# Performance work log

Hardware: AMD Instinct MI355X
Metric: run time of the kernel (lower is better)

The kernel has to match this reference:

```python
import jax, jax.numpy as jnp
import numpy as np

B = 128          # graphs
NPG = 512        # nodes per graph
N = B * NPG      # total nodes
DEG = 8
E = N * DEG      # total edges (intra-graph)
D = 100          # num_feature_dim / num_node_labels
HID = 128        # config.hidden
HEADS = 8
F1 = 20          # per-head dim of first GATConv in each GATNet
RATIO = 0.5
K = int(np.ceil(RATIO * NPG))  # nodes kept per graph by SAGPooling
NEG_SLOPE = 0.2


def setup_inputs() -> dict:
    key = jax.random.key(0)
    ks = jax.random.split(key, 24)
    x = jax.random.randint(ks[0], (N,), 0, D)
    # intra-graph random edges: local ids in [0, NPG) + graph offset
    src_l = jax.random.randint(ks[1], (B, NPG * DEG), 0, NPG)
    dst_l = jax.random.randint(ks[2], (B, NPG * DEG), 0, NPG)
    off = (jnp.arange(B) * NPG)[:, None]
    edge_index = jnp.stack([(src_l + off).ravel(), (dst_l + off).ravel()])
    batch = jnp.repeat(jnp.arange(B), NPG)

    def lin(k, fan_in, fan_out):
        return jax.random.normal(k, (fan_in, fan_out), jnp.float32) / np.sqrt(fan_in)

    def att(k, h, f):
        return jax.random.normal(k, (h, f), jnp.float32) * 0.1

    p = {
        # GATNet A (conv1): GATConv(D, 20, heads=8) then GATConv(160, HID, heads=1)
        "W_a1": lin(ks[3], D, HEADS * F1), "asrc_a1": att(ks[4], HEADS, F1),
        "adst_a1": att(ks[5], HEADS, F1), "b_a1": jnp.zeros((HEADS * F1,), jnp.float32),
        "W_a2": lin(ks[6], HEADS * F1, HID), "asrc_a2": att(ks[7], 1, HID),
        "adst_a2": att(ks[8], 1, HID), "b_a2": jnp.zeros((HID,), jnp.float32),
        # GATNet B (conv4): GATConv(HID, 20, heads=8) then GATConv(160, HID, heads=1)
        "W_b1": lin(ks[9], HID, HEADS * F1), "asrc_b1": att(ks[10], HEADS, F1),
        "adst_b1": att(ks[11], HEADS, F1), "b_b1": jnp.zeros((HEADS * F1,), jnp.float32),
        "W_b2": lin(ks[12], HEADS * F1, HID), "asrc_b2": att(ks[13], 1, HID),
        "adst_b2": att(ks[14], 1, HID), "b_b2": jnp.zeros((HID,), jnp.float32),
        # SAGPooling GraphConv(HID, 1)
        "w_rel": lin(ks[15], HID, 1), "w_root": lin(ks[16], HID, 1),
        "b_pool": jnp.zeros((1,), jnp.float32),
    }
    return {"x": x, "edge_index": edge_index, "batch": batch, **p}


def _gat_conv(h, src, dst, W, asrc, adst, b):
    """PyG GATConv (with self-loops already included in src/dst)."""
    Hh, Ff = asrc.shape
    z = (h @ W).reshape(N, Hh, Ff)                       # [N,H,F]
    es = jnp.sum(z * asrc, axis=-1)                      # [N,H] source logits
    ed = jnp.sum(z * adst, axis=-1)                      # [N,H] dest logits
    e = jax.nn.leaky_relu(es[src] + ed[dst], NEG_SLOPE)  # [E',H]
    m = jax.ops.segment_max(e, dst, num_segments=N)
    m = jnp.where(jnp.isfinite(m), m, 0.0)
    ex = jnp.exp(e - m[dst])
    den = jax.ops.segment_sum(ex, dst, num_segments=N)
    alpha = ex / (den[dst] + 1e-16)
    out = jax.ops.segment_sum(z[src] * alpha[:, :, None], dst, num_segments=N)
    return out.reshape(N, Hh * Ff) + b


def reference(x, edge_index, batch,
              W_a1, asrc_a1, adst_a1, b_a1, W_a2, asrc_a2, adst_a2, b_a2,
              W_b1, asrc_b1, adst_b1, b_b1, W_b2, asrc_b2, adst_b2, b_b2,
              w_rel, w_root, b_pool):
    src, dst = edge_index[0], edge_index[1]
    loops = jnp.arange(N)
    src_sl = jnp.concatenate([src, loops])  # GATConv adds self loops
    dst_sl = jnp.concatenate([dst, loops])

    h = jax.nn.one_hot(x, D, dtype=jnp.float32)
    # GATNet A: conv1 -> relu -> conv2 ; outer relu (dropout is eval no-op)
    h = jax.nn.relu(_gat_conv(h, src_sl, dst_sl, W_a1, asrc_a1, adst_a1, b_a1))
    h = _gat_conv(h, src_sl, dst_sl, W_a2, asrc_a2, adst_a2, b_a2)
    h = jax.nn.relu(h)
    # GATNet B
    h = jax.nn.relu(_gat_conv(h, src_sl, dst_sl, W_b1, asrc_b1, adst_b1, b_b1))
    h = _gat_conv(h, src_sl, dst_sl, W_b2, asrc_b2, adst_b2, b_b2)
    h = jax.nn.relu(h)

    # SAGPooling: GraphConv(HID,1) score (no self loops), tanh, per-graph top-k
    nbr = jax.ops.segment_sum(h[src], dst, num_segments=N)
    score = jnp.tanh(nbr @ w_rel + h @ w_root + b_pool).ravel()   # [N]
    sv, si = jax.lax.top_k(score.reshape(B, NPG), K)              # [B,K]
    perm = (si + (jnp.arange(B) * NPG)[:, None]).ravel()          # global node ids
    x_sel = h[perm] * sv.ravel()[:, None]                         # [B*K, HID]
    pooled = jnp.max(x_sel.reshape(B, K, HID), axis=1)            # global_max_pool
    batch_out = jnp.repeat(jnp.arange(B), K)
    return (pooled, perm, sv.ravel(), batch_out)
```

## Files before the change

kernel.cpp:

```cpp
#include <hip/hip_runtime.h>
#include <math.h>

#define N_NODES 65536
#define NPG     512
#define NGRAPH  128
#define E_EDGES 524288
#define MAXDEG  64
#define NHEADS  8
#define F1      20
#define HID     128
#define D160    160
#define KSEL    256
#define NLBL    100

#define IMG_A2_ELEMS (144*168)
#define IMG_B1_ELEMS (176*136)
#define PB_ZERO 0
#define PB_A2   64
#define PB_B1   (PB_A2 + 95)
#define PB_B2   (PB_B1 + 94)
#define PB_WA1  (PB_B2 + 95)
#define PB_EST  (PB_WA1 + 63)
#define PB_TOT  (PB_EST + 7)

typedef unsigned short ushort_t;
typedef unsigned int   uint_t;
typedef unsigned long long u64;
typedef __attribute__((ext_vector_type(8))) short short8;
typedef __attribute__((ext_vector_type(4))) float f32x4;

__device__ __forceinline__ float lrelu(float x){ return x > 0.f ? x : 0.2f*x; }
__device__ __forceinline__ ushort_t f2bf(float f){
    uint_t u = __float_as_uint(f);
    return (ushort_t)((u + 0x7FFFu + ((u >> 16) & 1u)) >> 16);
}
__device__ __forceinline__ float bf2f(ushort_t u){ return __uint_as_float(((uint_t)u) << 16); }
__device__ __forceinline__ float bflo(uint_t v){ return __uint_as_float(v << 16); }
__device__ __forceinline__ float bfhi(uint_t v){ return __uint_as_float(v & 0xFFFF0000u); }
__device__ __forceinline__ int xswz(int bid, int nblocks){
    return (bid & 7) * (nblocks >> 3) + (bid >> 3);
}
__device__ __forceinline__ float rdlanef(float v, int i){
    return __uint_as_float((uint_t)__builtin_amdgcn_readlane(__float_as_int(v), i));
}

__device__ __forceinline__ u64 comp_make(float s, int idx){
    uint_t u = __float_as_uint(s);
    u ^= (u & 0x80000000u) ? 0xFFFFFFFFu : 0x80000000u;
    return ((u64)u << 32) | (u64)(511 - idx);
}
__device__ __forceinline__ float comp_score(u64 c){
    uint_t u = (uint_t)(c >> 32);
    u ^= (u & 0x80000000u) ? 0x80000000u : 0xFFFFFFFFu;
    return __uint_as_float(u);
}
__device__ __forceinline__ int comp_idx(u64 c){ return 511 - (int)(c & 0x1FFu); }
__device__ __forceinline__ u64 shfl_xor_u64(u64 x, int m){
    uint_t lo = __shfl_xor((uint_t)x, m);
    uint_t hi = __shfl_xor((uint_t)(x >> 32), m);
    return ((u64)hi << 32) | lo;
}

__global__ void k_prep(const float* __restrict__ Wa1, const float* __restrict__ as1,
                       const float* __restrict__ ad1,
                       const float* __restrict__ Wa2, const float* __restrict__ as2,
                       const float* __restrict__ ad2,
                       const float* __restrict__ Wb1, const float* __restrict__ asb1,
                       const float* __restrict__ adb1,
                       const float* __restrict__ Wb2, const float* __restrict__ asb2,
                       const float* __restrict__ adb2,
                       int* __restrict__ deg,
                       ushort_t* __restrict__ imgA2, ushort_t* __restrict__ imgB1,
                       ushort_t* __restrict__ imgB2,
                       ushort_t* __restrict__ Wbf, float* __restrict__ esT,
                       float* __restrict__ edT){
    int bid = blockIdx.x, tid = threadIdx.x;
    if(bid < PB_A2){
        ((uint4*)deg)[(bid - PB_ZERO)*256 + tid] = (uint4){0,0,0,0};
    } else if(bid < PB_B1 || (bid >= PB_B2 && bid < PB_WA1)){
        bool isB2 = (bid >= PB_B2);
        int j = (bid - (isB2 ? PB_B2 : PB_A2))*256 + tid;
        if(j < IMG_A2_ELEMS){
            const float* W  = isB2 ? Wb2 : Wa2;
            const float* as = isB2 ? asb2 : as2;
            const float* ad = isB2 ? adb2 : ad2;
            int n = j / 168, k = j - n*168;
            float v = 0.f;
            if(k < 160){
                if(n < 128) v = W[k*128 + n];
                else if(n < 130){
                    const float* av = (n == 128) ? as : ad;
                    float s = 0.f;
                    for(int c=0; c<128; ++c) s += W[k*128 + c]*av[c];
                    v = s;
                }
            }
            (isB2 ? imgB2 : imgA2)[j] = f2bf(v);
        }
    } else if(bid < PB_B2){
        int j = (bid - PB_B1)*256 + tid;
        if(j < IMG_B1_ELEMS){
            int n = j / 136, k = j - n*136;
            float v = 0.f;
            if(k < 128){
                if(n < 160) v = Wb1[k*160 + n];
                else {
                    int j2 = n - 160, h = j2 & 7;
                    const float* av = ((j2 < 8) ? asb1 : adb1) + h*F1;
                    const float* wr = Wb1 + k*160 + h*F1;
                    float s = 0.f;
                    #pragma unroll
                    for(int f=0; f<F1; ++f) s += wr[f]*av[f];
                    v = s;
                }
            }
            imgB1[j] = f2bf(v);
        }
    } else if(bid < PB_EST){
        int j = (bid - PB_WA1)*256 + tid;
        if(j < NLBL*D160) Wbf[j] = f2bf(Wa1[j]);
    } else {
        int t = (bid - PB_EST)*256 + tid;
        if(t < NLBL*16){
            int lbl = t >> 4, j = t & 15, h = j & 7;
            const float* av = ((j < 8) ? as1 : ad1) + h*F1;
            const float* wr = Wa1 + lbl*D160 + h*F1;
            float s = 0.f;
            #pragma unroll
            for(int f=0; f<F1; ++f) s += wr[f]*av[f];
            if(j < 8) esT[lbl*8 + h] = s;
            else      edT[lbl*8 + h] = s;
        }
    }
}

__global__ void k_build_ell(const int* __restrict__ src, const int* __restrict__ dst,
                            int* __restrict__ deg, int* __restrict__ ell){
    int blk = xswz(blockIdx.x, E_EDGES/256);
    int e = blk*blockDim.x + threadIdx.x;
    int d = dst[e];
    int p = atomicAdd(&deg[d], 1);
    if(p < MAXDEG) ell[d*MAXDEG + p] = src[e];
}

__global__ __launch_bounds__(256) void k_attn8_a(const int* __restrict__ x,
        const int* __restrict__ deg, const int* __restrict__ ell,
        const ushort_t* __restrict__ Wbf, const float* __restrict__ esT,
        const float* __restrict__ edT, const float* __restrict__ bias,
        ushort_t* __restrict__ out){
    __shared__ __align__(16) ushort_t Wl[NLBL*D160];
    __shared__ float esL[NLBL*8], edL[NLBL*8];
    int tid = threadIdx.x;
    for(int i = tid; i < NLBL*D160/8; i += 256)
        ((uint4*)Wl)[i] = ((const uint4*)Wbf)[i];
    for(int i = tid; i < NLBL*8; i += 256){ esL[i] = esT[i]; edL[i] = edT[i]; }
    __syncthreads();
    int blk = xswz(blockIdx.x, N_NODES*NHEADS/256);
    int t = blk*256 + tid;
    int n = t >> 3, h = t & 7;
    int dg = deg[n]; if(dg > MAXDEG) dg = MAXDEG;
    int lbl = x[n];
    float edn = edL[lbl*8 + h];
    float wself = expf(lrelu(esL[lbl*8 + h] + edn));
    float den = wself;
    float acc[F1];
    {
        const uint_t* zn = (const uint_t*)Wl + lbl*80 + h*10;
        #pragma unroll
        for(int f=0; f<10; ++f){
            uint_t v = zn[f];
            acc[2*f]   = wself*bflo(v);
            acc[2*f+1] = wself*bfhi(v);
        }
    }
    const int* el = ell + n*MAXDEG;
    int i = 0;
    for(; i+2 <= dg; i += 2){
        int sa = el[i], sb = el[i+1];
        int la = x[sa], lb = x[sb];
        float wa = expf(lrelu(esL[la*8 + h] + edn));
        float wb = expf(lrelu(esL[lb*8 + h] + edn));
        den += wa + wb;
        const uint_t* za = (const uint_t*)Wl + la*80 + h*10;
        const uint_t* zb = (const uint_t*)Wl + lb*80 + h*10;
        #pragma unroll
        for(int f=0; f<10; ++f){
            uint_t va = za[f], vb = zb[f];
            acc[2*f]   += wa*bflo(va) + wb*bflo(vb);
            acc[2*f+1] += wa*bfhi(va) + wb*bfhi(vb);
        }
    }
    if(i < dg){
        int sa = el[i];
        int la = x[sa];
        float wa = expf(lrelu(esL[la*8 + h] + edn));
        den += wa;
        const uint_t* za = (const uint_t*)Wl + la*80 + h*10;
        #pragma unroll
        for(int f=0; f<10; ++f){
            uint_t va = za[f];
            acc[2*f]   += wa*bflo(va);
            acc[2*f+1] += wa*bfhi(va);
        }
    }
    float inv = 1.f/(den + 1e-16f);
    uint_t* o = (uint_t*)(out + (size_t)n*D160 + h*F1);
    const float* bb = bias + h*F1;
    #pragma unroll
    for(int f=0; f<10; ++f){
        float v0 = fmaxf(acc[2*f]*inv   + bb[2*f],   0.f);
        float v1 = fmaxf(acc[2*f+1]*inv + bb[2*f+1], 0.f);
        o[f] = (uint_t)f2bf(v0) | ((uint_t)f2bf(v1) << 16);
    }
}

__global__ void k_attn8(const int* __restrict__ deg, const int* __restrict__ ell,
                        const ushort_t* __restrict__ z8, const float* __restrict__ es8,
                        const float* __restrict__ ed8, const float* __restrict__ bias,
                        ushort_t* __restrict__ out){
    int blk = xswz(blockIdx.x, N_NODES*NHEADS/256);
    int t = blk*blockDim.x + threadIdx.x;
    int n = t >> 3, h = t & 7;
    int dg = deg[n]; if(dg > MAXDEG) dg = MAXDEG;
    float edn = ed8[t];
    float wself = expf(lrelu(es8[t] + edn));
    float den = wself;
    float acc[F1];
    const uint_t* zn = (const uint_t*)(z8 + (size_t)n*D160 + h*F1);
    #pragma unroll
    for(int f=0; f<10; ++f){
        uint_t v = zn[f];
        acc[2*f]   = wself*bflo(v);
        acc[2*f+1] = wself*bfhi(v);
    }
    const int* el = ell + n*MAXDEG;
    int i = 0;
    for(; i+2 <= dg; i += 2){
        int sa = el[i], sb = el[i+1];
        float ea = es8[sa*NHEADS + h], eb = es8[sb*NHEADS + h];
        const uint_t* za = (const uint_t*)(z8 + (size_t)sa*D160 + h*F1);
        const uint_t* zb = (const uint_t*)(z8 + (size_t)sb*D160 + h*F1);
        float wa = expf(lrelu(ea + edn));
        float wb = expf(lrelu(eb + edn));
        den += wa + wb;
        #pragma unroll
        for(int f=0; f<10; ++f){
            uint_t va = za[f], vb = zb[f];
            acc[2*f]   += wa*bflo(va) + wb*bflo(vb);
            acc[2*f+1] += wa*bfhi(va) + wb*bfhi(vb);
        }
    }
    if(i < dg){
        int sa = el[i];
        float ea = es8[sa*NHEADS + h];
        const uint_t* za = (const uint_t*)(z8 + (size_t)sa*D160 + h*F1);
        float wa = expf(lrelu(ea + edn));
        den += wa;
        #pragma unroll
        for(int f=0; f<10; ++f){
            uint_t va = za[f];
            acc[2*f]   += wa*bflo(va);
            acc[2*f+1] += wa*bfhi(va);
        }
    }
    float inv = 1.f/(den + 1e-16f);
    uint_t* o = (uint_t*)(out + (size_t)n*D160 + h*F1);
    const float* bb = bias + h*F1;
    #pragma unroll
    for(int f=0; f<10; ++f){
        float v0 = fmaxf(acc[2*f]*inv   + bb[2*f],   0.f);
        float v1 = fmaxf(acc[2*f+1]*inv + bb[2*f+1], 0.f);
        o[f] = (uint_t)f2bf(v0) | ((uint_t)f2bf(v1) << 16);
    }
}

template<int IN, int OUTC, int OUTIMG, bool ESED8>
__global__ __launch_bounds__(256) void k_gemm2(const ushort_t* __restrict__ Wimg,
                                               const ushort_t* __restrict__ A,
                                               ushort_t* __restrict__ C,
                                               float* __restrict__ oa,
                                               float* __restrict__ ob){
    constexpr int LDW = IN + 8;
    constexpr int NT = OUTIMG/16;
    constexpr int NC = OUTC/16;
    constexpr int KS = IN/32;
    constexpr int ELEMS = OUTIMG*LDW;
    __shared__ __align__(16) ushort_t Wt[ELEMS];
    int tid = threadIdx.x;
    int blk = xswz(blockIdx.x, N_NODES/64);
    int wave = tid >> 6, lane = tid & 63;
    int col16 = lane & 15;
    int kq = (lane >> 4) * 8;
    int row = blk*64 + wave*16 + col16;
    const ushort_t* Ar = A + (size_t)row*IN + kq;
    short8 afr[KS];
    #pragma unroll
    for(int ks=0; ks<KS; ++ks)
        afr[ks] = *reinterpret_cast<const short8*>(Ar + ks*32);
    for(int i = tid; i < ELEMS/8; i += 256)
        ((uint4*)Wt)[i] = ((const uint4*)Wimg)[i];
    __syncthreads();
    f32x4 acc[NT];
    #pragma unroll
    for(int c=0;c<NT;++c) acc[c] = (f32x4){0.f,0.f,0.f,0.f};
    #pragma unroll
    for(int ks=0; ks<KS; ++ks){
        #pragma unroll
        for(int c=0;c<NT;++c){
            short8 bf = *reinterpret_cast<const short8*>(&Wt[(c*16 + col16)*LDW + ks*32 + kq]);
            acc[c] = __builtin_amdgcn_mfma_f32_16x16x32_bf16(afr[ks], bf, acc[c], 0, 0, 0);
        }
    }
    int rbase = blk*64 + wave*16 + (lane >> 4)*4;
    #pragma unroll
    for(int c=0;c<NC;++c){
        #pragma unroll
        for(int r=0;r<4;++r){
            C[(size_t)(rbase + r)*OUTC + c*16 + col16] = f2bf(acc[c][r]);
        }
    }
    if(ESED8){
        #pragma unroll
        for(int r=0;r<4;++r){
            float v = acc[NT-1][r];
            if(col16 < 8) oa[(size_t)(rbase + r)*8 + col16] = v;
            else          ob[(size_t)(rbase + r)*8 + (col16 - 8)] = v;
        }
    } else {
        if(col16 == 0){
            #pragma unroll
            for(int r=0;r<4;++r) oa[rbase + r] = acc[NT-1][r];
        }
        if(col16 == 1){
            #pragma unroll
            for(int r=0;r<4;++r) ob[rbase + r] = acc[NT-1][r];
        }
    }
}

template<typename OutT, bool DOT>
__global__ void k_attn1(const int* __restrict__ deg, const int* __restrict__ ell,
                        const ushort_t* __restrict__ Z, const float* __restrict__ es,
                        const float* __restrict__ ed, const float* __restrict__ bias,
                        OutT* __restrict__ out,
                        const float* __restrict__ wa, const float* __restrict__ wb,
                        float* __restrict__ oa, float* __restrict__ ob){
    int blk = xswz(blockIdx.x, N_NODES/4);
    int gt = blk*blockDim.x + threadIdx.x;
    int n = gt >> 6;
    int l = threadIdx.x & 63;
    int dg = deg[n]; if(dg > MAXDEG) dg = MAXDEG;
    float edn = ed[n];
    float wself = expf(lrelu(es[n] + edn));
    int s_l = 0; float w_l = 0.f;
    if(l < dg){ s_l = ell[n*MAXDEG + l]; w_l = expf(lrelu(es[s_l] + edn)); }
    float den = w_l;
    for(int o=32;o>0;o>>=1) den += __shfl_xor(den,o);
    den += wself;
    const uint_t* Zu = (const uint_t*)Z;
    uint_t zn = Zu[(size_t)n*64 + l];
    float acc0 = wself*bflo(zn);
    float acc1 = wself*bfhi(zn);
    int i = 0;
    for(; i+4 <= dg; i += 4){
        int s0 = __builtin_amdgcn_readlane(s_l, i);
        int s1 = __builtin_amdgcn_readlane(s_l, i+1);
        int s2 = __builtin_amdgcn_readlane(s_l, i+2);
        int s3 = __builtin_amdgcn_readlane(s_l, i+3);
        uint_t z0 = Zu[(size_t)s0*64 + l];
        uint_t z1 = Zu[(size_t)s1*64 + l];
        uint_t z2 = Zu[(size_t)s2*64 + l];
        uint_t z3 = Zu[(size_t)s3*64 + l];
        float w0 = rdlanef(w_l, i);
        float w1 = rdlanef(w_l, i+1);
        float w2 = rdlanef(w_l, i+2);
        float w3 = rdlanef(w_l, i+3);
        acc0 += w0*bflo(z0) + w1*bflo(z1);
        acc1 += w0*bfhi(z0) + w1*bfhi(z1);
        acc0 += w2*bflo(z2) + w3*bflo(z3);
        acc1 += w2*bfhi(z2) + w3*bfhi(z3);
    }
    for(; i < dg; ++i){
        int s0 = __builtin_amdgcn_readlane(s_l, i);
        float w0 = rdlanef(w_l, i);
        uint_t z0 = Zu[(size_t)s0*64 + l];
        acc0 += w0*bflo(z0);
        acc1 += w0*bfhi(z0);
    }
    float inv = 1.f/(den + 1e-16f);
    float2 bb = ((const float2*)bias)[l];
    float r0 = fmaxf(acc0*inv + bb.x, 0.f);
    float r1 = fmaxf(acc1*inv + bb.y, 0.f);
    if(sizeof(OutT) == 2){
        ((uint_t*)out)[(size_t)n*64 + l] = (uint_t)f2bf(r0) | ((uint_t)f2bf(r1) << 16);
    } else {
        float2 rv; rv.x = r0; rv.y = r1;
        ((float2*)out)[(size_t)n*64 + l] = rv;
    }
    if(DOT){
        float2 a2 = ((const float2*)wa)[l];
        float2 b2 = ((const float2*)wb)[l];
        float pa = r0*a2.x + r1*a2.y;
        float pb = r0*b2.x + r1*b2.y;
        for(int o=32;o>0;o>>=1){ pa += __shfl_xor(pa,o); pb += __shfl_xor(pb,o); }
        if(l==0){ oa[n] = pa; ob[n] = pb; }
    }
}

__global__ void k_score(const int* __restrict__ deg, const int* __restrict__ ell,
                        const float* __restrict__ yrel, const float* __restrict__ rroot,
                        const float* __restrict__ bpool, float* __restrict__ score){
    int blk = xswz(blockIdx.x, N_NODES/256);
    int n = blk*blockDim.x + threadIdx.x;
    int dg = deg[n]; if(dg > MAXDEG) dg = MAXDEG;
    float s = rroot[n] + bpool[0];
    const int* el = ell + n*MAXDEG;
    int i = 0;
    for(; i+4 <= dg; i += 4){
        float y0 = yrel[el[i]],   y1 = yrel[el[i+1]];
        float y2 = yrel[el[i+2]], y3 = yrel[el[i+3]];
        s += (y0 + y1) + (y2 + y3);
    }
    for(; i < dg; ++i) s += yrel[el[i]];
    score[n] = tanhf(s);
}

__global__ __launch_bounds__(512) void k_topk_pool(const float* __restrict__ score,
                                                   const ushort_t* __restrict__ H,
                                                   float* __restrict__ pooled,
                                                   float* __restrict__ perm_f,
                                                   float* __restrict__ sv,
                                                   float* __restrict__ batch_f){
    __shared__ int   sidx[KSEL];
    __shared__ float sval[KSEL];
    __shared__ float pmax[512];
    int g = xswz(blockIdx.x, NGRAPH);
    int base = g*NPG;
    int t = threadIdx.x;
    if(t < 64){
        int l = t;
        u64 v[8];
        #pragma unroll
        for(int r=0;r<8;++r){
            int i = r*64 + l;
            v[r] = comp_make(score[base + i], i);
        }
        #pragma unroll
        for(int kk=1; kk<=9; ++kk){
            int k = 1 << kk;
            #pragma unroll
            for(int jj=kk-1; jj>=0; --jj){
                int j = 1 << jj;
                if(j < 64){
                    bool lower = (l & j) == 0;
                    #pragma unroll
                    for(int r=0;r<8;++r){
                        int i = r*64 + l;
                        u64 p = shfl_xor_u64(v[r], j);
                        bool desc = (i & k) == 0;
                        u64 mx = v[r] > p ? v[r] : p;
                        u64 mn = v[r] > p ? p : v[r];
                        v[r] = (lower == desc) ? mx : mn;
                    }
                } else {
                    int jr = j >> 6;
                    #pragma unroll
                    for(int r=0;r<8;++r){
                        if((r & jr) == 0){
                            int rp = r | jr;
                            int i = r*64 + l;
                            bool desc = (i & k) == 0;
                            u64 a = v[r], b = v[rp];
                            u64 mx = a > b ? a : b;
                            u64 mn = a > b ? b : a;
                            v[r]  = desc ? mx : mn;
                            v[rp] = desc ? mn : mx;
                        }
                    }
                }
            }
        }
        #pragma unroll
        for(int r=0;r<4;++r){
            int i = r*64 + l;
            int idx = comp_idx(v[r]);
            float s = comp_score(v[r]);
            perm_f[g*KSEL + i]  = (float)(base + idx);
            sv[g*KSEL + i]      = s;
            batch_f[g*KSEL + i] = (float)g;
            sidx[i] = idx; sval[i] = s;
        }
    }
    __syncthreads();
    int c = t & 127, kc = t >> 7;
    float mx = -1e30f;
    for(int kk = kc*64; kk < kc*64 + 64; ++kk){
        mx = fmaxf(mx, bf2f(H[(size_t)(base + sidx[kk])*HID + c]) * sval[kk]);
    }
    pmax[t] = mx;
    __syncthreads();
    if(t < HID){
        pooled[g*HID + t] = fmaxf(fmaxf(pmax[t], pmax[t+128]),
                                  fmaxf(pmax[t+256], pmax[t+384]));
    }
}

extern "C" void kernel_launch(void* const* d_in, const int* in_sizes, int n_in,
                              void* d_out, int out_size, void* d_ws, size_t ws_size,
                              hipStream_t stream) {
    const int*   x       = (const int*)  d_in[0];
    const int*   eidx    = (const int*)  d_in[1];
    const float* W_a1    = (const float*)d_in[3];
    const float* asrc_a1 = (const float*)d_in[4];
    const float* adst_a1 = (const float*)d_in[5];
    const float* b_a1    = (const float*)d_in[6];
    const float* W_a2    = (const float*)d_in[7];
    const float* asrc_a2 = (const float*)d_in[8];
    const float* adst_a2 = (const float*)d_in[9];
    const float* b_a2    = (const float*)d_in[10];
    const float* W_b1    = (const float*)d_in[11];
    const float* asrc_b1 = (const float*)d_in[12];
    const float* adst_b1 = (const float*)d_in[13];
    const float* b_b1    = (const float*)d_in[14];
    const float* W_b2    = (const float*)d_in[15];
    const float* asrc_b2 = (const float*)d_in[16];
    const float* adst_b2 = (const float*)d_in[17];
    const float* b_b2    = (const float*)d_in[18];
    const float* w_rel   = (const float*)d_in[19];
    const float* w_root  = (const float*)d_in[20];
    const float* b_pool  = (const float*)d_in[21];

    const int* e_src = eidx;
    const int* e_dst = eidx + E_EDGES;

    char* ws = (char*)d_ws;
    size_t off = 0;
    auto alloc = [&](size_t bytes)->char*{
        char* p = ws + off;
        off += (bytes + 255) & ~(size_t)255;
        return p;
    };
    int*      deg    = (int*)     alloc((size_t)N_NODES*4);
    int*      ell    = (int*)     alloc((size_t)N_NODES*MAXDEG*4);
    ushort_t* z8     = (ushort_t*)alloc((size_t)N_NODES*D160*2);
    ushort_t* h8     = (ushort_t*)alloc((size_t)N_NODES*D160*2);
    ushort_t* zc     = (ushort_t*)alloc((size_t)N_NODES*HID*2);
    ushort_t* hmid   = (ushort_t*)alloc((size_t)N_NODES*HID*2);
    ushort_t* hfin   = (ushort_t*)alloc((size_t)N_NODES*HID*2);
    float*    es8    = (float*)   alloc((size_t)N_NODES*NHEADS*4);
    float*    ed8    = (float*)   alloc((size_t)N_NODES*NHEADS*4);
    float*    es1    = (float*)   alloc((size_t)N_NODES*4);
    float*    ed1    = (float*)   alloc((size_t)N_NODES*4);
    float*    yrel   = (float*)   alloc((size_t)N_NODES*4);
    float*    rroot  = (float*)   alloc((size_t)N_NODES*4);
    float*    score  = (float*)   alloc((size_t)N_NODES*4);
    ushort_t* Wbf    = (ushort_t*)alloc((size_t)NLBL*D160*2);
    float*    esT    = (float*)   alloc((size_t)NLBL*8*4);
    float*    edT    = (float*)   alloc((size_t)NLBL*8*4);
    ushort_t* imgA2  = (ushort_t*)alloc((size_t)IMG_A2_ELEMS*2);
    ushort_t* imgB1  = (ushort_t*)alloc((size_t)IMG_B1_ELEMS*2);
    ushort_t* imgB2  = (ushort_t*)alloc((size_t)IMG_A2_ELEMS*2);
    (void)ws_size; (void)n_in; (void)in_sizes; (void)out_size;

    float* out      = (float*)d_out;
    float* pooled   = out;
    float* perm_f   = out + NGRAPH*HID;
    float* sv       = perm_f + NGRAPH*KSEL;
    float* batch_f  = sv + NGRAPH*KSEL;

    k_prep<<<PB_TOT, 256, 0, stream>>>(W_a1, asrc_a1, adst_a1,
                                       W_a2, asrc_a2, adst_a2,
                                       W_b1, asrc_b1, adst_b1,
                                       W_b2, asrc_b2, adst_b2,
                                       deg, imgA2, imgB1, imgB2, Wbf, esT, edT);
    k_build_ell<<<E_EDGES/256, 256, 0, stream>>>(e_src, e_dst, deg, ell);

    k_attn8_a<<<N_NODES*NHEADS/256, 256, 0, stream>>>(x, deg, ell, Wbf, esT, edT, b_a1, h8);

    k_gemm2<D160, HID, 144, false><<<N_NODES/64, 256, 0, stream>>>(imgA2, h8, zc, es1, ed1);
    k_attn1<ushort_t, false><<<N_NODES/4, 256, 0, stream>>>(deg, ell, zc, es1, ed1, b_a2, hmid,
                                                            nullptr, nullptr, nullptr, nullptr);

    k_gemm2<HID, D160, 176, true><<<N_NODES/64, 256, 0, stream>>>(imgB1, hmid, z8, es8, ed8);
    k_attn8<<<N_NODES*NHEADS/256, 256, 0, stream>>>(deg, ell, z8, es8, ed8, b_b1, h8);

    k_gemm2<D160, HID, 144, false><<<N_NODES/64, 256, 0, stream>>>(imgB2, h8, zc, es1, ed1);
    k_attn1<ushort_t, true><<<N_NODES/4, 256, 0, stream>>>(deg, ell, zc, es1, ed1, b_b2, hfin,
                                                           w_rel, w_root, yrel, rroot);

    k_score<<<N_NODES/256, 256, 0, stream>>>(deg, ell, yrel, rroot, b_pool, score);
    k_topk_pool<<<NGRAPH, NPG, 0, stream>>>(score, hfin, pooled, perm_f, sv, batch_f);
}
```

Baseline: 226.4 us.

## Stage per-graph node features in LDS for the attention aggregation kernels

The per-head and single-head GAT aggregation kernels now give each block one graph and one half of the feature channels. The block loads that graph's 512 node feature rows and attention logits into shared memory, and neighbour gathers then read LDS instead of scattered global memory. This relies on every edge staying inside its graph, which the task's input construction guarantees; neighbour ids are masked to a local index. The channel split means the SAGPool dot products become two partial sums, which the score kernel adds back together. In exchange, only 256 large blocks run (about one per CU), the 8-head kernel holds 80 accumulators per thread, and each node's neighbour loop runs serially, so occupancy drops and register spills are possible.

```diff
diff --git a/kernel.cpp b/kernel.cpp
--- a/kernel.cpp
+++ b/kernel.cpp
@@ -39,9 +39,6 @@
 __device__ __forceinline__ float bfhi(uint_t v){ return __uint_as_float(v & 0xFFFF0000u); }
 __device__ __forceinline__ int xswz(int bid, int nblocks){
     return (bid & 7) * (nblocks >> 3) + (bid >> 3);
-}
-__device__ __forceinline__ float rdlanef(float v, int i){
-    return __uint_as_float((uint_t)__builtin_amdgcn_readlane(__float_as_int(v), i));
 }
 
 __device__ __forceinline__ u64 comp_make(float s, int idx){
@@ -214,63 +211,88 @@
     }
 }
 
-__global__ void k_attn8(const int* __restrict__ deg, const int* __restrict__ ell,
-                        const ushort_t* __restrict__ z8, const float* __restrict__ es8,
-                        const float* __restrict__ ed8, const float* __restrict__ bias,
-                        ushort_t* __restrict__ out){
-    int blk = xswz(blockIdx.x, N_NODES*NHEADS/256);
-    int t = blk*blockDim.x + threadIdx.x;
-    int n = t >> 3, h = t & 7;
-    int dg = deg[n]; if(dg > MAXDEG) dg = MAXDEG;
-    float edn = ed8[t];
-    float wself = expf(lrelu(es8[t] + edn));
-    float den = wself;
-    float acc[F1];
-    const uint_t* zn = (const uint_t*)(z8 + (size_t)n*D160 + h*F1);
+__global__ __launch_bounds__(512) void k_attn8b(const int* __restrict__ deg,
+        const int* __restrict__ ell, const ushort_t* __restrict__ z8,
+        const float* __restrict__ es8, const float* __restrict__ ed8,
+        const float* __restrict__ bias, ushort_t* __restrict__ out){
+    __shared__ __align__(16) ushort_t zl[512*88];
+    __shared__ __align__(16) float4 esl[512];
+    __shared__ __align__(16) float4 edl[512];
+    int tid = threadIdx.x;
+    int blk = xswz(blockIdx.x, NGRAPH*2);
+    int g = blk >> 1, hg = blk & 1;
+    int base = g*NPG;
+    for(int idx = tid; idx < 512*10; idx += 512){
+        int row = idx/10, q = idx - (idx/10)*10;
+        uint4 v = *(const uint4*)(z8 + (size_t)(base+row)*D160 + hg*80 + q*8);
+        *(uint4*)(zl + row*88 + q*8) = v;
+    }
+    esl[tid] = *(const float4*)(es8 + (size_t)(base+tid)*8 + hg*4);
+    edl[tid] = *(const float4*)(ed8 + (size_t)(base+tid)*8 + hg*4);
+    __syncthreads();
+    int n = tid;
+    int dg = deg[base+n]; if(dg > MAXDEG) dg = MAXDEG;
+    const int* el = ell + (size_t)(base+n)*MAXDEG;
+    float4 edn = edl[n];
+    float4 esn = esl[n];
+    float w0 = expf(lrelu(esn.x + edn.x));
+    float w1 = expf(lrelu(esn.y + edn.y));
+    float w2 = expf(lrelu(esn.z + edn.z));
+    float w3 = expf(lrelu(esn.w + edn.w));
+    float den0 = w0, den1 = w1, den2 = w2, den3 = w3;
+    float acc[80];
     #pragma unroll
-    for(int f=0; f<10; ++f){
-        uint_t v = zn[f];
-        acc[2*f]   = wself*bflo(v);
-        acc[2*f+1] = wself*bfhi(v);
-    }
-    const int* el = ell + n*MAXDEG;
-    int i = 0;
-    for(; i+2 <= dg; i += 2){
-        int sa = el[i], sb = el[i+1];
-        float ea = es8[sa*NHEADS + h], eb = es8[sb*NHEADS + h];
-        const uint_t* za = (const uint_t*)(z8 + (size_t)sa*D160 + h*F1);
-        const uint_t* zb = (const uint_t*)(z8 + (size_t)sb*D160 + h*F1);
-        float wa = expf(lrelu(ea + edn));
-        float wb = expf(lrelu(eb + edn));
-        den += wa + wb;
-        #pragma unroll
-        for(int f=0; f<10; ++f){
-            uint_t va = za[f], vb = zb[f];
-            acc[2*f]   += wa*bflo(va) + wb*bflo(vb);
-            acc[2*f+1] += wa*bfhi(va) + wb*bfhi(vb);
-        }
-    }
-    if(i < dg){
-        int sa = el[i];
-        float ea = es8[sa*NHEADS + h];
-        const uint_t* za = (const uint_t*)(z8 + (size_t)sa*D160 + h*F1);
-        float wa = expf(lrelu(ea + edn));
-        den += wa;
-        #pragma unroll
-        for(int f=0; f<10; ++f){
-            uint_t va = za[f];
-            acc[2*f]   += wa*bflo(va);
-            acc[2*f+1] += wa*bfhi(va);
-        }
-    }
-    float inv = 1.f/(den + 1e-16f);
-    uint_t* o = (uint_t*)(out + (size_t)n*D160 + h*F1);
-    const float* bb = bias + h*F1;
+    for(int q=0; q<10; ++q){
+        uint4 v = *(const uint4*)(zl + n*88 + q*8);
+        const uint_t* vu = (const uint_t*)&v;
+        #pragma unroll
+        for(int r=0; r<4; ++r){
+            int ch = q*8 + r*2;
+            float wA = (ch < 20) ? w0 : (ch < 40) ? w1 : (ch < 60) ? w2 : w3;
+            float wB = (ch+1 < 20) ? w0 : (ch+1 < 40) ? w1 : (ch+1 < 60) ? w2 : w3;
+            acc[ch]   = wA*bflo(vu[r]);
+            acc[ch+1] = wB*bfhi(vu[r]);
+        }
+    }
+    for(int i=0; i<dg; ++i){
+        int s = el[i] & (NPG-1);
+        float4 es_s = esl[s];
+        float wa0 = expf(lrelu(es_s.x + edn.x));
+        float wa1 = expf(lrelu(es_s.y + edn.y));
+        float wa2 = expf(lrelu(es_s.z + edn.z));
+        float wa3 = expf(lrelu(es_s.w + edn.w));
+        den0 += wa0; den1 += wa1; den2 += wa2; den3 += wa3;
+        #pragma unroll
+        for(int q=0; q<10; ++q){
+            uint4 v = *(const uint4*)(zl + s*88 + q*8);
+            const uint_t* vu = (const uint_t*)&v;
+            #pragma unroll
+            for(int r=0; r<4; ++r){
+                int ch = q*8 + r*2;
+                float wA = (ch < 20) ? wa0 : (ch < 40) ? wa1 : (ch < 60) ? wa2 : wa3;
+                float wB = (ch+1 < 20) ? wa0 : (ch+1 < 40) ? wa1 : (ch+1 < 60) ? wa2 : wa3;
+                acc[ch]   += wA*bflo(vu[r]);
+                acc[ch+1] += wB*bfhi(vu[r]);
+            }
+        }
+    }
+    float inv0 = 1.f/(den0 + 1e-16f);
+    float inv1 = 1.f/(den1 + 1e-16f);
+    float inv2 = 1.f/(den2 + 1e-16f);
+    float inv3 = 1.f/(den3 + 1e-16f);
+    const float* bb = bias + hg*80;
+    uint_t* o = (uint_t*)out + (size_t)(base+n)*80 + hg*40;
     #pragma unroll
-    for(int f=0; f<10; ++f){
-        float v0 = fmaxf(acc[2*f]*inv   + bb[2*f],   0.f);
-        float v1 = fmaxf(acc[2*f+1]*inv + bb[2*f+1], 0.f);
-        o[f] = (uint_t)f2bf(v0) | ((uint_t)f2bf(v1) << 16);
+    for(int q=0; q<10; ++q){
+        #pragma unroll
+        for(int r=0; r<4; ++r){
+            int ch = q*8 + r*2;
+            float iA = (ch < 20) ? inv0 : (ch < 40) ? inv1 : (ch < 60) ? inv2 : inv3;
+            float iB = (ch+1 < 20) ? inv0 : (ch+1 < 40) ? inv1 : (ch+1 < 60) ? inv2 : inv3;
+            float v0 = fmaxf(acc[ch]*iA   + bb[ch],   0.f);
+            float v1 = fmaxf(acc[ch+1]*iB + bb[ch+1], 0.f);
+            o[q*4 + r] = (uint_t)f2bf(v0) | ((uint_t)f2bf(v1) << 16);
+        }
     }
 }
 
@@ -338,90 +360,88 @@
     }
 }
 
-template<typename OutT, bool DOT>
-__global__ void k_attn1(const int* __restrict__ deg, const int* __restrict__ ell,
-                        const ushort_t* __restrict__ Z, const float* __restrict__ es,
-                        const float* __restrict__ ed, const float* __restrict__ bias,
-                        OutT* __restrict__ out,
-                        const float* __restrict__ wa, const float* __restrict__ wb,
-                        float* __restrict__ oa, float* __restrict__ ob){
-    int blk = xswz(blockIdx.x, N_NODES/4);
-    int gt = blk*blockDim.x + threadIdx.x;
-    int n = gt >> 6;
-    int l = threadIdx.x & 63;
-    int dg = deg[n]; if(dg > MAXDEG) dg = MAXDEG;
-    float edn = ed[n];
-    float wself = expf(lrelu(es[n] + edn));
-    int s_l = 0; float w_l = 0.f;
-    if(l < dg){ s_l = ell[n*MAXDEG + l]; w_l = expf(lrelu(es[s_l] + edn)); }
-    float den = w_l;
-    for(int o=32;o>0;o>>=1) den += __shfl_xor(den,o);
-    den += wself;
-    const uint_t* Zu = (const uint_t*)Z;
-    uint_t zn = Zu[(size_t)n*64 + l];
-    float acc0 = wself*bflo(zn);
-    float acc1 = wself*bfhi(zn);
-    int i = 0;
-    for(; i+4 <= dg; i += 4){
-        int s0 = __builtin_amdgcn_readlane(s_l, i);
-        int s1 = __builtin_amdgcn_readlane(s_l, i+1);
-        int s2 = __builtin_amdgcn_readlane(s_l, i+2);
-        int s3 = __builtin_amdgcn_readlane(s_l, i+3);
-        uint_t z0 = Zu[(size_t)s0*64 + l];
-        uint_t z1 = Zu[(size_t)s1*64 + l];
-        uint_t z2 = Zu[(size_t)s2*64 + l];
-        uint_t z3 = Zu[(size_t)s3*64 + l];
-        float w0 = rdlanef(w_l, i);
-        float w1 = rdlanef(w_l, i+1);
-        float w2 = rdlanef(w_l, i+2);
-        float w3 = rdlanef(w_l, i+3);
-        acc0 += w0*bflo(z0) + w1*bflo(z1);
-        acc1 += w0*bfhi(z0) + w1*bfhi(z1);
-        acc0 += w2*bflo(z2) + w3*bflo(z3);
-        acc1 += w2*bfhi(z2) + w3*bfhi(z3);
-    }
-    for(; i < dg; ++i){
-        int s0 = __builtin_amdgcn_readlane(s_l, i);
-        float w0 = rdlanef(w_l, i);
-        uint_t z0 = Zu[(size_t)s0*64 + l];
-        acc0 += w0*bflo(z0);
-        acc1 += w0*bfhi(z0);
-    }
-    float inv = 1.f/(den + 1e-16f);
-    float2 bb = ((const float2*)bias)[l];
-    float r0 = fmaxf(acc0*inv + bb.x, 0.f);
-    float r1 = fmaxf(acc1*inv + bb.y, 0.f);
-    if(sizeof(OutT) == 2){
-        ((uint_t*)out)[(size_t)n*64 + l] = (uint_t)f2bf(r0) | ((uint_t)f2bf(r1) << 16);
-    } else {
-        float2 rv; rv.x = r0; rv.y = r1;
-        ((float2*)out)[(size_t)n*64 + l] = rv;
-    }
-    if(DOT){
-        float2 a2 = ((const float2*)wa)[l];
-        float2 b2 = ((const float2*)wb)[l];
-        float pa = r0*a2.x + r1*a2.y;
-        float pb = r0*b2.x + r1*b2.y;
-        for(int o=32;o>0;o>>=1){ pa += __shfl_xor(pa,o); pb += __shfl_xor(pb,o); }
-        if(l==0){ oa[n] = pa; ob[n] = pb; }
+template<bool DOT>
+__global__ __launch_bounds__(512) void k_attn1L(const int* __restrict__ deg,
+        const int* __restrict__ ell, const ushort_t* __restrict__ Z,
+        const float* __restrict__ es, const float* __restrict__ ed,
+        const float* __restrict__ bias, ushort_t* __restrict__ out,
+        const float* __restrict__ wa, const float* __restrict__ wb,
+        float* __restrict__ oa, float* __restrict__ ob){
+    __shared__ __align__(16) ushort_t zl[512*72];
+    __shared__ float esl[512], edl[512];
+    int tid = threadIdx.x;
+    int blk = xswz(blockIdx.x, NGRAPH*2);
+    int g = blk >> 1, cc = blk & 1;
+    int base = g*NPG;
+    for(int idx = tid; idx < 512*8; idx += 512){
+        int row = idx >> 3, q = idx & 7;
+        *(uint4*)(zl + row*72 + q*8) =
+            *(const uint4*)(Z + (size_t)(base+row)*HID + cc*64 + q*8);
+    }
+    esl[tid] = es[base+tid];
+    edl[tid] = ed[base+tid];
+    __syncthreads();
+    int wv = tid >> 6, l = tid & 63;
+    int half = l >> 5, lc = l & 31;
+    for(int it=0; it<32; ++it){
+        int n = wv*64 + it*2 + half;
+        int dgn = deg[base+n]; if(dgn > MAXDEG) dgn = MAXDEG;
+        float edn = edl[n];
+        float wself = expf(lrelu(esl[n] + edn));
+        float den = wself;
+        uint_t zn = *(const uint_t*)(zl + n*72 + lc*2);
+        float a0 = wself*bflo(zn);
+        float a1 = wself*bfhi(zn);
+        const int* el = ell + (size_t)(base+n)*MAXDEG;
+        for(int i=0; i<dgn; ++i){
+            int s = el[i] & (NPG-1);
+            float w = expf(lrelu(esl[s] + edn));
+            den += w;
+            uint_t zv = *(const uint_t*)(zl + s*72 + lc*2);
+            a0 += w*bflo(zv);
+            a1 += w*bfhi(zv);
+        }
+        float inv = 1.f/(den + 1e-16f);
+        float2 bb = ((const float2*)(bias + cc*64))[lc];
+        float r0 = fmaxf(a0*inv + bb.x, 0.f);
+        float r1 = fmaxf(a1*inv + bb.y, 0.f);
+        ((uint_t*)out)[(size_t)(base+n)*64 + cc*32 + lc] =
+            (uint_t)f2bf(r0) | ((uint_t)f2bf(r1) << 16);
+        if(DOT){
+            float2 a2 = ((const float2*)(wa + cc*64))[lc];
+            float2 b2 = ((const float2*)(wb + cc*64))[lc];
+            float pa = r0*a2.x + r1*a2.y;
+            float pb = r0*b2.x + r1*b2.y;
+            for(int o=16; o>0; o>>=1){ pa += __shfl_xor(pa,o); pb += __shfl_xor(pb,o); }
+            if(lc == 0){
+                oa[cc*N_NODES + base + n] = pa;
+                ob[cc*N_NODES + base + n] = pb;
+            }
+        }
     }
 }
 
 __global__ void k_score(const int* __restrict__ deg, const int* __restrict__ ell,
-                        const float* __restrict__ yrel, const float* __restrict__ rroot,
+                        const float* __restrict__ y2, const float* __restrict__ r2,
                         const float* __restrict__ bpool, float* __restrict__ score){
     int blk = xswz(blockIdx.x, N_NODES/256);
     int n = blk*blockDim.x + threadIdx.x;
     int dg = deg[n]; if(dg > MAXDEG) dg = MAXDEG;
-    float s = rroot[n] + bpool[0];
+    float s = r2[n] + r2[N_NODES + n] + bpool[0];
     const int* el = ell + n*MAXDEG;
     int i = 0;
     for(; i+4 <= dg; i += 4){
-        float y0 = yrel[el[i]],   y1 = yrel[el[i+1]];
-        float y2 = yrel[el[i+2]], y3 = yrel[el[i+3]];
-        s += (y0 + y1) + (y2 + y3);
-    }
-    for(; i < dg; ++i) s += yrel[el[i]];
+        int e0 = el[i], e1 = el[i+1], e2 = el[i+2], e3 = el[i+3];
+        float y0 = y2[e0] + y2[N_NODES + e0];
+        float y1 = y2[e1] + y2[N_NODES + e1];
+        float ya = y2[e2] + y2[N_NODES + e2];
+        float yb = y2[e3] + y2[N_NODES + e3];
+        s += (y0 + y1) + (ya + yb);
+    }
+    for(; i < dg; ++i){
+        int e0 = el[i];
+        s += y2[e0] + y2[N_NODES + e0];
+    }
     score[n] = tanhf(s);
 }
 
@@ -551,8 +571,8 @@
     float*    ed8    = (float*)   alloc((size_t)N_NODES*NHEADS*4);
     float*    es1    = (float*)   alloc((size_t)N_NODES*4);
     float*    ed1    = (float*)   alloc((size_t)N_NODES*4);
-    float*    yrel   = (float*)   alloc((size_t)N_NODES*4);
-    float*    rroot  = (float*)   alloc((size_t)N_NODES*4);
+    float*    yrel2  = (float*)   alloc((size_t)N_NODES*2*4);
+    float*    rroot2 = (float*)   alloc((size_t)N_NODES*2*4);
     float*    score  = (float*)   alloc((size_t)N_NODES*4);
     ushort_t* Wbf    = (ushort_t*)alloc((size_t)NLBL*D160*2);
     float*    esT    = (float*)   alloc((size_t)NLBL*8*4);
@@ -578,16 +598,16 @@
     k_attn8_a<<<N_NODES*NHEADS/256, 256, 0, stream>>>(x, deg, ell, Wbf, esT, edT, b_a1, h8);
 
     k_gemm2<D160, HID, 144, false><<<N_NODES/64, 256, 0, stream>>>(imgA2, h8, zc, es1, ed1);
-    k_attn1<ushort_t, false><<<N_NODES/4, 256, 0, stream>>>(deg, ell, zc, es1, ed1, b_a2, hmid,
-                                                            nullptr, nullptr, nullptr, nullptr);
+    k_attn1L<false><<<NGRAPH*2, 512, 0, stream>>>(deg, ell, zc, es1, ed1, b_a2, hmid,
+                                                  nullptr, nullptr, nullptr, nullptr);
 
     k_gemm2<HID, D160, 176, true><<<N_NODES/64, 256, 0, stream>>>(imgB1, hmid, z8, es8, ed8);
-    k_attn8<<<N_NODES*NHEADS/256, 256, 0, stream>>>(deg, ell, z8, es8, ed8, b_b1, h8);
+    k_attn8b<<<NGRAPH*2, 512, 0, stream>>>(deg, ell, z8, es8, ed8, b_b1, h8);
 
     k_gemm2<D160, HID, 144, false><<<N_NODES/64, 256, 0, stream>>>(imgB2, h8, zc, es1, ed1);
-    k_attn1<ushort_t, true><<<N_NODES/4, 256, 0, stream>>>(deg, ell, zc, es1, ed1, b_b2, hfin,
-                                                           w_rel, w_root, yrel, rroot);
-
-    k_score<<<N_NODES/256, 256, 0, stream>>>(deg, ell, yrel, rroot, b_pool, score);
+    k_attn1L<true><<<NGRAPH*2, 512, 0, stream>>>(deg, ell, zc, es1, ed1, b_b2, hfin,
+                                                 w_rel, w_root, yrel2, rroot2);
+
+    k_score<<<N_NODES/256, 256, 0, stream>>>(deg, ell, yrel2, rroot2, b_pool, score);
     k_topk_pool<<<NGRAPH, NPG, 0, stream>>>(score, hfin, pooled, perm_f, sv, batch_f);
 }
```

Result: slower. 303.4 us (+34.0%).

## Stage per-graph z8 features in shared memory for 8-head attention aggregation

Applied to the files above, without the earlier changes.

Replaces the per-(node,head) attention kernel for the second GATNet's first conv with a per-graph kernel: each block loads half the heads (4 of 8) of one graph's 512 nodes' features and scores into LDS, then each thread aggregates its node's neighbours from LDS. This exploits the fact that edges are intra-graph, turning scattered global gathers into shared-memory reads. The trade-offs are fewer blocks (256), a large LDS footprint (~106 KB per block), 80 accumulators per thread with high register pressure, and a dependence on edges never leaving their graph.

```diff
diff --git a/kernel.cpp b/kernel.cpp
--- a/kernel.cpp
+++ b/kernel.cpp
@@ -214,63 +214,88 @@
     }
 }
 
-__global__ void k_attn8(const int* __restrict__ deg, const int* __restrict__ ell,
-                        const ushort_t* __restrict__ z8, const float* __restrict__ es8,
-                        const float* __restrict__ ed8, const float* __restrict__ bias,
-                        ushort_t* __restrict__ out){
-    int blk = xswz(blockIdx.x, N_NODES*NHEADS/256);
-    int t = blk*blockDim.x + threadIdx.x;
-    int n = t >> 3, h = t & 7;
-    int dg = deg[n]; if(dg > MAXDEG) dg = MAXDEG;
-    float edn = ed8[t];
-    float wself = expf(lrelu(es8[t] + edn));
-    float den = wself;
-    float acc[F1];
-    const uint_t* zn = (const uint_t*)(z8 + (size_t)n*D160 + h*F1);
+__global__ __launch_bounds__(512) void k_attn8b(const int* __restrict__ deg,
+        const int* __restrict__ ell, const ushort_t* __restrict__ z8,
+        const float* __restrict__ es8, const float* __restrict__ ed8,
+        const float* __restrict__ bias, ushort_t* __restrict__ out){
+    __shared__ __align__(16) ushort_t zl[512*88];
+    __shared__ __align__(16) float4 esl[512];
+    __shared__ __align__(16) float4 edl[512];
+    int tid = threadIdx.x;
+    int blk = xswz(blockIdx.x, NGRAPH*2);
+    int g = blk >> 1, hg = blk & 1;
+    int base = g*NPG;
+    for(int idx = tid; idx < 512*10; idx += 512){
+        int row = idx/10, q = idx - (idx/10)*10;
+        uint4 v = *(const uint4*)(z8 + (size_t)(base+row)*D160 + hg*80 + q*8);
+        *(uint4*)(zl + row*88 + q*8) = v;
+    }
+    esl[tid] = *(const float4*)(es8 + (size_t)(base+tid)*8 + hg*4);
+    edl[tid] = *(const float4*)(ed8 + (size_t)(base+tid)*8 + hg*4);
+    __syncthreads();
+    int n = tid;
+    int dg = deg[base+n]; if(dg > MAXDEG) dg = MAXDEG;
+    const int* el = ell + (size_t)(base+n)*MAXDEG;
+    float4 edn = edl[n];
+    float4 esn = esl[n];
+    float w0 = expf(lrelu(esn.x + edn.x));
+    float w1 = expf(lrelu(esn.y + edn.y));
+    float w2 = expf(lrelu(esn.z + edn.z));
+    float w3 = expf(lrelu(esn.w + edn.w));
+    float den0 = w0, den1 = w1, den2 = w2, den3 = w3;
+    float acc[80];
     #pragma unroll
-    for(int f=0; f<10; ++f){
-        uint_t v = zn[f];
-        acc[2*f]   = wself*bflo(v);
-        acc[2*f+1] = wself*bfhi(v);
-    }
-    const int* el = ell + n*MAXDEG;
-    int i = 0;
-    for(; i+2 <= dg; i += 2){
-        int sa = el[i], sb = el[i+1];
-        float ea = es8[sa*NHEADS + h], eb = es8[sb*NHEADS + h];
-        const uint_t* za = (const uint_t*)(z8 + (size_t)sa*D160 + h*F1);
-        const uint_t* zb = (const uint_t*)(z8 + (size_t)sb*D160 + h*F1);
-        float wa = expf(lrelu(ea + edn));
-        float wb = expf(lrelu(eb + edn));
-        den += wa + wb;
-        #pragma unroll
-        for(int f=0; f<10; ++f){
-            uint_t va = za[f], vb = zb[f];
-            acc[2*f]   += wa*bflo(va) + wb*bflo(vb);
-            acc[2*f+1] += wa*bfhi(va) + wb*bfhi(vb);
-        }
-    }
-    if(i < dg){
-        int sa = el[i];
-        float ea = es8[sa*NHEADS + h];
-        const uint_t* za = (const uint_t*)(z8 + (size_t)sa*D160 + h*F1);
-        float wa = expf(lrelu(ea + edn));
-        den += wa;
-        #pragma unroll
-        for(int f=0; f<10; ++f){
-            uint_t va = za[f];
-            acc[2*f]   += wa*bflo(va);
-            acc[2*f+1] += wa*bfhi(va);
-        }
-    }
-    float inv = 1.f/(den + 1e-16f);
-    uint_t* o = (uint_t*)(out + (size_t)n*D160 + h*F1);
-    const float* bb = bias + h*F1;
+    for(int q=0; q<10; ++q){
+        uint4 v = *(const uint4*)(zl + n*88 + q*8);
+        const uint_t* vu = (const uint_t*)&v;
+        #pragma unroll
+        for(int r=0; r<4; ++r){
+            int ch = q*8 + r*2;
+            float wA = (ch < 20) ? w0 : (ch < 40) ? w1 : (ch < 60) ? w2 : w3;
+            float wB = (ch+1 < 20) ? w0 : (ch+1 < 40) ? w1 : (ch+1 < 60) ? w2 : w3;
+            acc[ch]   = wA*bflo(vu[r]);
+            acc[ch+1] = wB*bfhi(vu[r]);
+        }
+    }
+    for(int i=0; i<dg; ++i){
+        int s = el[i] & (NPG-1);
+        float4 es_s = esl[s];
+        float wa0 = expf(lrelu(es_s.x + edn.x));
+        float wa1 = expf(lrelu(es_s.y + edn.y));
+        float wa2 = expf(lrelu(es_s.z + edn.z));
+        float wa3 = expf(lrelu(es_s.w + edn.w));
+        den0 += wa0; den1 += wa1; den2 += wa2; den3 += wa3;
+        #pragma unroll
+        for(int q=0; q<10; ++q){
+            uint4 v = *(const uint4*)(zl + s*88 + q*8);
+            const uint_t* vu = (const uint_t*)&v;
+            #pragma unroll
+            for(int r=0; r<4; ++r){
+                int ch = q*8 + r*2;
+                float wA = (ch < 20) ? wa0 : (ch < 40) ? wa1 : (ch < 60) ? wa2 : wa3;
+                float wB = (ch+1 < 20) ? wa0 : (ch+1 < 40) ? wa1 : (ch+1 < 60) ? wa2 : wa3;
+                acc[ch]   += wA*bflo(vu[r]);
+                acc[ch+1] += wB*bfhi(vu[r]);
+            }
+        }
+    }
+    float inv0 = 1.f/(den0 + 1e-16f);
+    float inv1 = 1.f/(den1 + 1e-16f);
+    float inv2 = 1.f/(den2 + 1e-16f);
+    float inv3 = 1.f/(den3 + 1e-16f);
+    const float* bb = bias + hg*80;
+    uint_t* o = (uint_t*)out + (size_t)(base+n)*80 + hg*40;
     #pragma unroll
-    for(int f=0; f<10; ++f){
-        float v0 = fmaxf(acc[2*f]*inv   + bb[2*f],   0.f);
-        float v1 = fmaxf(acc[2*f+1]*inv + bb[2*f+1], 0.f);
-        o[f] = (uint_t)f2bf(v0) | ((uint_t)f2bf(v1) << 16);
+    for(int q=0; q<10; ++q){
+        #pragma unroll
+        for(int r=0; r<4; ++r){
+            int ch = q*8 + r*2;
+            float iA = (ch < 20) ? inv0 : (ch < 40) ? inv1 : (ch < 60) ? inv2 : inv3;
+            float iB = (ch+1 < 20) ? inv0 : (ch+1 < 40) ? inv1 : (ch+1 < 60) ? inv2 : inv3;
+            float v0 = fmaxf(acc[ch]*iA   + bb[ch],   0.f);
+            float v1 = fmaxf(acc[ch+1]*iB + bb[ch+1], 0.f);
+            o[q*4 + r] = (uint_t)f2bf(v0) | ((uint_t)f2bf(v1) << 16);
+        }
     }
 }
 
@@ -582,7 +607,7 @@
                                                             nullptr, nullptr, nullptr, nullptr);
 
     k_gemm2<HID, D160, 176, true><<<N_NODES/64, 256, 0, stream>>>(imgB1, hmid, z8, es8, ed8);
-    k_attn8<<<N_NODES*NHEADS/256, 256, 0, stream>>>(deg, ell, z8, es8, ed8, b_b1, h8);
+    k_attn8b<<<NGRAPH*2, 512, 0, stream>>>(deg, ell, z8, es8, ed8, b_b1, h8);
 
     k_gemm2<D160, HID, 144, false><<<N_NODES/64, 256, 0, stream>>>(imgB2, h8, zc, es1, ed1);
     k_attn1<ushort_t, true><<<N_NODES/4, 256, 0, stream>>>(deg, ell, zc, es1, ed1, b_b2, hfin,
```

Measured after the change: 226.2 us. No clear change (-0.1%).
